# Optimization experiments

Hardware: AMD Instinct MI355X
Metric: run time of the kernel (lower is better)

## Reference

```python
import jax, jax.numpy as jnp
import numpy as np

B, T, C, H, W = 2, 8, 4, 128, 128
P = 8; D = 128; DEPTH = 2; E = 4; HD = 2 * D
Hp, Wp = H // P, W // P; F2 = 2 * D; CPP = C * P * P


def _ln(x, g, b):
    m = x.mean(-1, keepdims=True)
    v = ((x - m) ** 2).mean(-1, keepdims=True)
    return (x - m) * jax.lax.rsqrt(v + 1e-5) * g + b


def setup_inputs():
    key = jax.random.key(0)
    it = iter(jax.random.split(key, 32))
    def n(shape, s=0.02):
        return jax.random.normal(next(it), shape, jnp.float32) * s
    z = lambda shape: jnp.zeros(shape, jnp.float32)
    return {
        "x": jax.random.normal(next(it), (B, T, C, H, W), jnp.float32),
        "dt": jax.random.uniform(next(it), (T,), jnp.float32, 0.1, 1.0),
        "enc_Wre": n((CPP, D)), "enc_Wim": n((CPP, D)),
        "dec_W": n((F2, CPP)), "dec_b": z((CPP,)),
        "ln_sp_g": jnp.ones((DEPTH, F2), jnp.float32), "ln_sp_b": z((DEPTH, F2)),
        "conv_W": n((DEPTH, F2, F2, 3, 3), 0.05), "conv_b": z((DEPTH, F2)),
        "E_re": n((DEPTH, D, D), 0.05), "E_im": n((DEPTH, D, D), 0.05),
        "Dc_re": n((DEPTH, D, D), 0.05), "Dc_im": n((DEPTH, D, D), 0.05),
        "gate_W": n((DEPTH, F2, D)), "gate_b": z((DEPTH, D)),
        "src_W": n((DEPTH, F2, F2)), "src_b": z((DEPTH, F2)),
        "flux_decay": z((DEPTH, D)),
        "lam_re": n((DEPTH, D), 0.5), "lam_im": n((DEPTH, D), 0.5),
        "ln_t_g": jnp.ones((DEPTH, F2), jnp.float32), "ln_t_b": z((DEPTH, F2)),
        "rtr_W": n((DEPTH, F2, E)),
        "W1": n((DEPTH, E, F2, HD)), "b1": z((DEPTH, E, HD)),
        "W2": n((DEPTH, E, HD, F2)), "b2": z((DEPTH, E, F2)),
    }


def _forward(x, dt, enc_Wre, enc_Wim, dec_W, dec_b, ln_sp_g, ln_sp_b, conv_W, conv_b,
             E_re, E_im, Dc_re, Dc_im, gate_W, gate_b, src_W, src_b, flux_decay,
             lam_re, lam_im, ln_t_g, ln_t_b, rtr_W, W1, b1, W2, b2):
    Bx, Tx = x.shape[:2]
    # patch-embed encoder -> complex latent [B,T,D,Hp,Wp]
    f = x.reshape(Bx, Tx, C, Hp, P, Wp, P).transpose(0, 1, 3, 5, 2, 4, 6).reshape(Bx, Tx, Hp, Wp, CPP)
    zc = (f @ enc_Wre) + 1j * (f @ enc_Wim)
    zc = zc.transpose(0, 1, 4, 2, 3)
    dtBT = jnp.broadcast_to(dt[None, :], (Bx, Tx))
    flux = jnp.zeros((Bx, D), jnp.complex64)
    for i in range(DEPTH):
        # spatial branch: LayerNorm over [re,im] channels + Clifford-style 3x3 conv
        zr = jnp.concatenate([zc.real, zc.imag], axis=2).reshape(Bx * Tx, F2, Hp, Wp)
        xn = _ln(zr.transpose(0, 2, 3, 1), ln_sp_g[i], ln_sp_b[i]).transpose(0, 3, 1, 2)
        xs = jax.lax.conv_general_dilated(xn, conv_W[i], (1, 1), 'SAME',
                                          dimension_numbers=('NCHW', 'OIHW', 'NCHW')) + conv_b[i][None, :, None, None]
        sre, sim = jnp.split(xs, 2, axis=1)
        zc = zc + (sre + 1j * sim).reshape(Bx, Tx, D, Hp, Wp)
        # eigen-basis encode (complex channel mixing)
        xe = zc.transpose(0, 1, 3, 4, 2) @ (E_re[i] + 1j * E_im[i])  # B,T,Hp,Wp,D
        xm = xe.mean(axis=(2, 3))  # B,T,D complex
        # sequential flux tracker: inherently recurrent -> lax.scan over T
        gW, gb, sW, sb = gate_W[i], gate_b[i], src_W[i], src_b[i]
        dec = jax.nn.sigmoid(flux_decay[i])
        def step(fl, xmt):
            inp = jnp.concatenate([xmt.real, xmt.imag], -1)
            gate = jax.nn.sigmoid(inp @ gW + gb)
            s2 = inp @ sW + sb
            src = s2[..., :D] + 1j * s2[..., D:]
            fn = dec * fl + gate * xmt + (1.0 - gate) * src
            return fn, (fn, src)
        flux, (flux_seq, src_seq) = jax.lax.scan(step, flux, xm.transpose(1, 0, 2))
        flux_seq = flux_seq.transpose(1, 0, 2)
        src_seq = src_seq.transpose(1, 0, 2)
        g = jax.nn.sigmoid(jnp.concatenate([flux_seq.real, flux_seq.imag], -1) @ gW + gb)[:, :, None, None, :]
        forcing = xe * g + src_seq[:, :, None, None, :] * (1.0 - g)
        # complex transition operators (ZOH-style discretization)
        lam = -jax.nn.softplus(lam_re[i]) + 1j * lam_im[i]  # [D]
        opd = jnp.exp(dtBT[:, :, None] * lam[None, None, :])  # B,T,D complex
        opf = (opd - 1.0) / lam
        u = forcing * opf[:, :, None, None, :]
        A = jnp.broadcast_to(opd[:, :, None, None, :], u.shape)
        def comb(a, b):
            aA, aX = a
            bA, bX = b
            return (aA * bA, bX + bA * aX)
        # parallel pscan over time: h_t = A_t*h_{t-1} + u_t, independent per (B,Hp,Wp)
        _, uo = jax.lax.associative_scan(comb, (A, u), axis=1)
        xo = uo @ (Dc_re[i] + 1j * Dc_im[i])  # basis decode, B,T,Hp,Wp,D
        xon = _ln(jnp.concatenate([xo.real, xo.imag], -1), ln_t_g[i], ln_t_b[i])
        xcc = xon[..., :D] + 1j * xon[..., D:]
        # MoE FFN with soft routing over experts
        ft = jnp.concatenate([xcc.real, xcc.imag], -1).reshape(-1, F2)  # [M,2D]
        gates = jax.nn.softmax(ft @ rtr_W[i], axis=-1)  # [M,E]
        hmid = jax.nn.gelu(jnp.einsum('mf,efh->emh', ft, W1[i]) + b1[i][:, None, :])
        oexp = jnp.einsum('emh,ehf->emf', hmid, W2[i]) + b2[i][:, None, :]
        dtok = jnp.einsum('me,emf->mf', gates, oexp).reshape(Bx, Tx, Hp, Wp, F2)
        delta = dtok[..., :D] + 1j * dtok[..., D:]
        zc = zc + (xcc + delta).transpose(0, 1, 4, 2, 3)
    # decoder: project [re,im] -> pixels and unpatchify (real output)
    zl = zc.transpose(0, 1, 3, 4, 2)
    fo = jnp.concatenate([zl.real, zl.imag], -1) @ dec_W + dec_b
    return fo.reshape(Bx, Tx, Hp, Wp, C, P, P).transpose(0, 1, 4, 2, 5, 3, 6).reshape(Bx, Tx, C, H, W)


def reference(x, dt, enc_Wre, enc_Wim, dec_W, dec_b, ln_sp_g, ln_sp_b, conv_W, conv_b,
              E_re, E_im, Dc_re, Dc_im, gate_W, gate_b, src_W, src_b, flux_decay,
              lam_re, lam_im, ln_t_g, ln_t_b, rtr_W, W1, b1, W2, b2):
    return _forward(x, dt, enc_Wre, enc_Wim, dec_W, dec_b, ln_sp_g, ln_sp_b, conv_W, conv_b,
                    E_re, E_im, Dc_re, Dc_im, gate_W, gate_b, src_W, src_b, flux_decay,
                    lam_re, lam_im, ln_t_g, ln_t_b, rtr_W, W1, b1, W2, b2)
```

## Files before the change

### kernel.cpp

```cpp
#include <hip/hip_runtime.h>
#include <hip/hip_bf16.h>
#include <math.h>


#define NIN 28
typedef unsigned short u16;
typedef __attribute__((ext_vector_type(8))) short bf16x8;
typedef __attribute__((ext_vector_type(4))) float f32x4;
typedef __attribute__((ext_vector_type(8))) unsigned short us8;

__device__ __forceinline__ float b2f(u16 u){ union{unsigned i;float f;}v; v.i=((unsigned)u)<<16; return v.f; }
__device__ __forceinline__ u16 f2b(float x){ __hip_bfloat16 h=__float2bfloat16(x); return *(u16*)&h; }
__device__ __forceinline__ float loadraw(const void* p, size_t i, int bf){
  return bf? b2f(((const u16*)p)[i]) : ((const float*)p)[i];
}
__device__ __forceinline__ int bfflag(const void* p){ return *(const unsigned*)p==0x3F803F80u; }
__device__ __forceinline__ float d_sigmoid(float x){ return 1.0f/(1.0f+expf(-x)); }
__device__ __forceinline__ float d_softplus(float x){ return fmaxf(x,0.0f)+log1pf(expf(-fabsf(x))); }
__device__ __forceinline__ float d_gelu(float x){
  const float c=0.7978845608028654f;
  return 0.5f*x*(1.0f+tanhf(c*(x+0.044715f*x*x*x)));
}

#define NF32 17
struct MP {
  const void* src[NIN];
  int f32dst[NF32]; int f32cum[NF32+1];
  int seg[6];
};

__global__ __launch_bounds__(256) void mega_prep(MP a, float* __restrict__ W,
    u16* __restrict__ encB, u16* __restrict__ decB, u16* __restrict__ convB,
    u16* __restrict__ cplxB, u16* __restrict__ w1B, u16* __restrict__ w2c){
  const int bf=bfflag(a.src[6]);
  const int tid=threadIdx.x;
  if(blockIdx.x<512){
    __shared__ float lds[2304];
    int io=blockIdx.x;
    size_t base=(size_t)io*2304;
    for(int r=tid;r<2304;r+=256) lds[r]=loadraw(a.src[8], base+r, bf);
    __syncthreads();
    for(int k=tid;k<2304;k+=256){
      int ic=k&255, kg=k>>8;
      convB[base+k]=f2b(lds[ic*9+kg]);
    }
    return;
  }
  int g=(blockIdx.x-512)*256+tid;
  if(g>=a.seg[5]) return;
  if(g<a.seg[0]){
    int i=0;
    while(i<NF32-1 && g>=a.f32cum[i+1]) i++;
    int local=g-a.f32cum[i];
    const int needs[NF32]={1,5,6,7,9,14,15,16,17,18,19,20,21,22,23,25,27};
    W[a.f32dst[i]+local]=loadraw(a.src[needs[i]], local, bf);
  } else if(g<a.seg[1]){
    int idx=g-a.seg[0]; int n=idx>>8, k=idx&255;
    float v=(n<128)? loadraw(a.src[2],(size_t)k*128+n,bf) : loadraw(a.src[3],(size_t)k*128+(n-128),bf);
    encB[idx]=f2b(v);
  } else if(g<a.seg[2]){
    int idx=g-a.seg[1]; int n=idx>>8, k=idx&255;
    decB[idx]=f2b(loadraw(a.src[4],(size_t)k*256+n,bf));
  } else if(g<a.seg[3]){
    int idx=g-a.seg[2];
    int mat=idx>>16; int r=idx&65535; int n=r>>8, k=r&255;
    int depth=mat&1; int isD=mat>>1;
    const void* re=isD? a.src[12]:a.src[10];
    const void* im=isD? a.src[13]:a.src[11];
    size_t base=(size_t)depth*16384;
    float v;
    if(k<128){ v = (n<128)? loadraw(re,base+(size_t)k*128+n,bf) : loadraw(im,base+(size_t)k*128+(n-128),bf); }
    else{ int kk=k-128;
      v = (n<128)? -loadraw(im,base+(size_t)kk*128+n,bf) : loadraw(re,base+(size_t)kk*128+(n-128),bf); }
    cplxB[idx]=f2b(v);
  } else if(g<a.seg[4]){
    int idx=g-a.seg[3]; int m=idx>>16; int r=idx&65535; int n=r>>8, k=r&255;
    w1B[idx]=f2b(loadraw(a.src[24],(size_t)m*65536+(size_t)k*256+n,bf));
  } else {
    int idx=g-a.seg[4];
    int i=idx>>18; int r=idx&262143; int n=r>>10; int k=r&1023;
    int e=k>>8, h=k&255;
    size_t s=(((size_t)(i*4+e)*256+h)*256+n);
    w2c[idx]=f2b(loadraw(a.src[26],s,bf));
  }
}

#define FB_BIAS 1
#define FB_GELU 2
#define FB_RS 4
#define FB_ADDTO 8
#define FB_WF32 16
#define FB_WBF16 32
#define FB_CONV 64
#define FB_MOE2 256
#define FB_UNPATCH 512
#define FB_XM 1024

template<int FLAGS>
__global__ __launch_bounds__(256,4) void mfma_gemm(
    const void* __restrict__ Asrc, const u16* __restrict__ Bt,
    const float* __restrict__ bias, const float* __restrict__ gates,
    float* __restrict__ Cf, u16* __restrict__ Cb,
    const u16* __restrict__ Xtra, void* __restrict__ Cout, const void* __restrict__ flagp,
    int K, long aE, long bE, long biasE, long cE, long cRow,
    float* __restrict__ xm4)
{
  __shared__ u16 As[2][64][72];
  __shared__ u16 Bs[2][64][72];
  const int e=blockIdx.z;
  const u16* A=(const u16*)Asrc + (size_t)e*aE;
  Bt += (size_t)e*bE;
  const float* biasp = bias? bias+(size_t)e*biasE : nullptr;
  const int bn=blockIdx.x*64, bm=blockIdx.y*64;
  const int tid=threadIdx.x, l=tid&63, w=tid>>6;
  const int wm=w&1, wn=w>>1;
  int bf=0;
  if(FLAGS&FB_UNPATCH) bf=bfflag(flagp);
  const us8 z8={0,0,0,0,0,0,0,0};

  auto loadAi=[&](int k0, int i)->us8{
    int c=tid+(i<<8); int row=c>>3, col8=(c&7)<<3;
    int gk=k0+col8;
    if(FLAGS&FB_CONV){
      int m=bm+row; int bt=m>>8, rem=m&255, hp=rem>>4, wp=rem&15;
      int kg=gk>>8, ic=gk&255; int ky=kg/3, kx=kg-3*ky;
      int y=hp+ky-1, x=wp+kx-1;
      return ((unsigned)y<16u && (unsigned)x<16u)?
           *(const us8*)&A[(((size_t)(bt*16+y))*16+x)*256+ic] : z8;
    }
    return *(const us8*)&A[(size_t)(bm+row)*K+gk];
  };
  auto loadBi=[&](int k0, int i)->us8{
    int c=tid+(i<<8); int row=c>>3, col8=(c&7)<<3;
    return *(const us8*)&Bt[(size_t)(bn+row)*K+k0+col8];
  };

  us8 ra0,ra1,rb0,rb1;
  ra0=loadAi(0,0); ra1=loadAi(0,1); rb0=loadBi(0,0); rb1=loadBi(0,1);
  {
    int c0=tid, c1=tid+256;
    *(us8*)&As[0][c0>>3][(c0&7)<<3]=ra0;
    *(us8*)&As[0][c1>>3][(c1&7)<<3]=ra1;
    *(us8*)&Bs[0][c0>>3][(c0&7)<<3]=rb0;
    *(us8*)&Bs[0][c1>>3][(c1&7)<<3]=rb1;
  }
  const int kSteps=K>>6;
  if(kSteps>1){ ra0=loadAi(64,0); ra1=loadAi(64,1); rb0=loadBi(64,0); rb1=loadBi(64,1); }
  __syncthreads();

  f32x4 zf={0.f,0.f,0.f,0.f};
  f32x4 acc00=zf, acc01=zf, acc10=zf, acc11=zf;
  const int aRow0=wm*32+(l&15), bRow0=wn*32+(l&15);
  const int kcL=(l>>4)<<3;

  for(int ks=0; ks<kSteps; ++ks){
    const int cur=ks&1;
    if(ks+1<kSteps){
      int nb=cur^1;
      int c0=tid, c1=tid+256;
      *(us8*)&As[nb][c0>>3][(c0&7)<<3]=ra0;
      *(us8*)&As[nb][c1>>3][(c1&7)<<3]=ra1;
      *(us8*)&Bs[nb][c0>>3][(c0&7)<<3]=rb0;
      *(us8*)&Bs[nb][c1>>3][(c1&7)<<3]=rb1;
      if(ks+2<kSteps){
        int k0=(ks+2)<<6;
        ra0=loadAi(k0,0); ra1=loadAi(k0,1); rb0=loadBi(k0,0); rb1=loadBi(k0,1);
      }
    }
    #pragma unroll
    for(int kk=0;kk<64;kk+=32){
      const int kc=kk+kcL;
      bf16x8 a0=*(const bf16x8*)&As[cur][aRow0   ][kc];
      bf16x8 a1=*(const bf16x8*)&As[cur][aRow0+16][kc];
      bf16x8 b0=*(const bf16x8*)&Bs[cur][bRow0   ][kc];
      bf16x8 b1=*(const bf16x8*)&Bs[cur][bRow0+16][kc];
      acc00=__builtin_amdgcn_mfma_f32_16x16x32_bf16(a0,b0,acc00,0,0,0);
      acc01=__builtin_amdgcn_mfma_f32_16x16x32_bf16(a0,b1,acc01,0,0,0);
      acc10=__builtin_amdgcn_mfma_f32_16x16x32_bf16(a1,b0,acc10,0,0,0);
      acc11=__builtin_amdgcn_mfma_f32_16x16x32_bf16(a1,b1,acc11,0,0,0);
    }
    __syncthreads();
  }

  const int rr=(l>>4)<<2, cc=l&15;
  #pragma unroll
  for(int mi=0;mi<2;mi++){
    #pragma unroll
    for(int ni=0;ni<2;ni++){
      f32x4 av = mi? (ni?acc11:acc10) : (ni?acc01:acc00);
      #pragma unroll
      for(int r=0;r<4;r++){
        int m=bm+wm*32+mi*16+rr+r;
        int n=bn+wn*32+ni*16+cc;
        float v=av[r];
        if(FLAGS&FB_BIAS) v+=biasp[n];
        if(FLAGS&FB_GELU) v=d_gelu(v);
        if(FLAGS&FB_RS)   v*=gates[(size_t)m*4+e];
        if(FLAGS&FB_MOE2){
          #pragma unroll
          for(int ee=0;ee<4;ee++) v+=gates[(size_t)m*4+ee]*bias[ee*256+n];
          v+=b2f(Xtra[(size_t)m*256+n]);
        }
        if(FLAGS&FB_UNPATCH){
          int bt=m>>8, hp=(m>>4)&15, wp=m&15;
          int c=n>>6, ph=(n>>3)&7, pw=n&7;
          size_t o=((size_t)bt<<16)|((size_t)c<<14)|((size_t)(hp*8+ph)<<7)|(size_t)(wp*8+pw);
          if(bf) ((__hip_bfloat16*)Cout)[o]=__float2bfloat16(v);
          else   ((float*)Cout)[o]=v;
          continue;
        }
        size_t o=(size_t)e*cE + (size_t)m*cRow + n;
        if(FLAGS&FB_ADDTO) v+=Cf[o];
        if(FLAGS&(FB_WF32|FB_ADDTO)) Cf[o]=v;
        if(FLAGS&FB_WBF16) Cb[o]=f2b(v);
      }
    }
  }

  if(FLAGS&FB_XM){
    float cs0=acc00[0]+acc00[1]+acc00[2]+acc00[3] + acc10[0]+acc10[1]+acc10[2]+acc10[3];
    float cs1=acc01[0]+acc01[1]+acc01[2]+acc01[3] + acc11[0]+acc11[1]+acc11[2]+acc11[3];
    cs0+=__shfl_xor(cs0,16); cs0+=__shfl_xor(cs0,32);
    cs1+=__shfl_xor(cs1,16); cs1+=__shfl_xor(cs1,32);
    float* xr=(float*)&As[0][0][0];
    if(l<16){
      xr[wm*64 + wn*32 + cc]      = cs0;
      xr[wm*64 + wn*32 + 16 + cc] = cs1;
    }
    __syncthreads();
    if(tid<64){
      float s=xr[tid]+xr[64+tid];
      xm4[(size_t)blockIdx.y*256 + bn + tid]=s;
    }
  }
}

#define FR_GATHER 1
#define FR_WF32 2
#define FR_MOE2 4
#define FR_ADDTO 8
#define FR_LN 16
#define FR_RTR 32

template<int FLAGS>
__global__ __launch_bounds__(256) void gemm_fullrow(
    const void* __restrict__ Asrc, const u16* __restrict__ Bt,
    const float* __restrict__ b2, const float* __restrict__ gatesIn,
    float* __restrict__ Cf, const u16* __restrict__ Xtra,
    const float* __restrict__ lnG, const float* __restrict__ lnB, u16* __restrict__ lnOut,
    const float* __restrict__ rtr, float* __restrict__ gatesOut,
    const void* __restrict__ flagp, int K)
{
  __shared__ u16 As[2][16][72];
  __shared__ u16 Bs[2][256][72];
  __shared__ float sc[480];
  const int bm=blockIdx.x*16;
  const int tid=threadIdx.x, l=tid&63, w=tid>>6;
  int bf=0;
  if(FLAGS&FR_GATHER) bf=bfflag(flagp);
  const bool aAct = tid<128;

  auto loadA=[&](int k0)->us8{
    int row=tid>>3, col8=(tid&7)<<3;
    int gk=k0+col8;
    if(FLAGS&FR_GATHER){
      int m=bm+row; int bt=m>>8, rem=m&255, hp=rem>>4, wp=rem&15;
      int c2=gk>>6, ph=(gk>>3)&7;
      size_t sidx=(((size_t)bt*4+c2)<<14)+(size_t)((hp*8+ph)<<7)+wp*8;
      if(bf) return *(const us8*)&((const u16*)Asrc)[sidx];
      const float* xf=(const float*)Asrc+sidx;
      us8 t;
      #pragma unroll
      for(int j=0;j<8;j++) t[j]=f2b(xf[j]);
      return t;
    }
    return *(const us8*)&((const u16*)Asrc)[(size_t)(bm+row)*K+gk];
  };
  auto loadB=[&](int k0, int j)->us8{
    int c=tid+(j<<8); int row=c>>3, col8=(c&7)<<3;
    return *(const us8*)&Bt[(size_t)row*K+k0+col8];
  };

  us8 ra, rb[8];
  if(aAct) ra=loadA(0);
  #pragma unroll
  for(int j=0;j<8;j++) rb[j]=loadB(0,j);
  if(aAct) *(us8*)&As[0][tid>>3][(tid&7)<<3]=ra;
  #pragma unroll
  for(int j=0;j<8;j++){ int c=tid+(j<<8); *(us8*)&Bs[0][c>>3][(c&7)<<3]=rb[j]; }
  const int kSteps=K>>6;
  if(kSteps>1){ if(aAct) ra=loadA(64); 
    #pragma unroll
    for(int j=0;j<8;j++) rb[j]=loadB(64,j); }
  __syncthreads();

  f32x4 zf={0.f,0.f,0.f,0.f};
  f32x4 acc[4]={zf,zf,zf,zf};
  const int kcL=(l>>4)<<3;

  for(int ks=0; ks<kSteps; ++ks){
    const int cur=ks&1;
    if(ks+1<kSteps){
      int nb=cur^1;
      if(aAct) *(us8*)&As[nb][tid>>3][(tid&7)<<3]=ra;
      #pragma unroll
      for(int j=0;j<8;j++){ int c=tid+(j<<8); *(us8*)&Bs[nb][c>>3][(c&7)<<3]=rb[j]; }
      if(ks+2<kSteps){
        int k0=(ks+2)<<6;
        if(aAct) ra=loadA(k0);
        #pragma unroll
        for(int j=0;j<8;j++) rb[j]=loadB(k0,j);
      }
    }
    #pragma unroll
    for(int kk=0;kk<64;kk+=32){
      const int kc=kk+kcL;
      bf16x8 a=*(const bf16x8*)&As[cur][l&15][kc];
      #pragma unroll
      for(int ni=0;ni<4;ni++){
        bf16x8 b=*(const bf16x8*)&Bs[cur][w*64+ni*16+(l&15)][kc];
        acc[ni]=__builtin_amdgcn_mfma_f32_16x16x32_bf16(a,b,acc[ni],0,0,0);
      }
    }
    __syncthreads();
  }

  const int rr=(l>>4)<<2, cc=l&15;
  float v[4][4];
  #pragma unroll
  for(int ni=0;ni<4;ni++){
    #pragma unroll
    for(int r=0;r<4;r++){
      int m=bm+rr+r, n=w*64+ni*16+cc;
      float x=acc[ni][r];
      if(FLAGS&FR_MOE2){
        #pragma unroll
        for(int ee=0;ee<4;ee++) x+=gatesIn[(size_t)m*4+ee]*b2[ee*256+n];
        x+=b2f(Xtra[(size_t)m*256+n]);
      }
      size_t o=(size_t)m*256+n;
      if(FLAGS&FR_ADDTO) x+=Cf[o];
      if(FLAGS&(FR_WF32|FR_ADDTO)) Cf[o]=x;
      v[ni][r]=x;
    }
  }

  if(FLAGS&FR_LN){
    float rs[4]={0,0,0,0}, rq[4]={0,0,0,0};
    #pragma unroll
    for(int ni=0;ni<4;ni++)
      #pragma unroll
      for(int r=0;r<4;r++){ rs[r]+=v[ni][r]; rq[r]+=v[ni][r]*v[ni][r]; }
    #pragma unroll
    for(int o=1;o<16;o<<=1){
      #pragma unroll
      for(int r=0;r<4;r++){ rs[r]+=__shfl_xor(rs[r],o); rq[r]+=__shfl_xor(rq[r],o); }
    }
    if((l&15)==0){
      int q=l>>4;
      #pragma unroll
      for(int r=0;r<4;r++){ sc[w*16+q*4+r]=rs[r]; sc[64+w*16+q*4+r]=rq[r]; }
    }
    __syncthreads();
    if(tid<16){
      float tot=0,tq=0;
      #pragma unroll
      for(int w4=0;w4<4;w4++){ tot+=sc[w4*16+tid]; tq+=sc[64+w4*16+tid]; }
      float mean=tot*(1.0f/256.0f);
      float var=tq*(1.0f/256.0f)-mean*mean;
      sc[128+tid]=mean; sc[144+tid]=rsqrtf(var+1e-5f);
    }
    __syncthreads();
    float nvv[4][4];
    #pragma unroll
    for(int ni=0;ni<4;ni++)
      #pragma unroll
      for(int r=0;r<4;r++){
        int row=rr+r, n=w*64+ni*16+cc;
        float nv=(v[ni][r]-sc[128+row])*sc[144+row]*lnG[n]+lnB[n];
        nvv[ni][r]=nv;
        lnOut[(size_t)(bm+row)*256+n]=f2b(nv);
      }
    if(FLAGS&FR_RTR){
      float pe[4][4]={{0,0,0,0},{0,0,0,0},{0,0,0,0},{0,0,0,0}};
      #pragma unroll
      for(int ni=0;ni<4;ni++){
        int n=w*64+ni*16+cc;
        #pragma unroll
        for(int r=0;r<4;r++)
          #pragma unroll
          for(int e=0;e<4;e++) pe[r][e]+=nvv[ni][r]*rtr[n*4+e];
      }
      #pragma unroll
      for(int o=1;o<16;o<<=1)
        #pragma unroll
        for(int r=0;r<4;r++)
          #pragma unroll
          for(int e=0;e<4;e++) pe[r][e]+=__shfl_xor(pe[r][e],o);
      if((l&15)==0){
        int q=l>>4;
        #pragma unroll
        for(int r=0;r<4;r++)
          #pragma unroll
          for(int e=0;e<4;e++) sc[160+w*64+(q*4+r)*4+e]=pe[r][e];
      }
      __syncthreads();
      if(tid<64){
        int row=tid>>2, e=tid&3;
        float t=0;
        #pragma unroll
        for(int w4=0;w4<4;w4++) t+=sc[160+w4*64+row*4+e];
        sc[416+row*4+e]=t;
      }
      __syncthreads();
      if(tid<16){
        float a0=sc[416+tid*4],a1=sc[416+tid*4+1],a2=sc[416+tid*4+2],a3=sc[416+tid*4+3];
        float mx=fmaxf(fmaxf(a0,a1),fmaxf(a2,a3));
        float e0=expf(a0-mx),e1=expf(a1-mx),e2=expf(a2-mx),e3=expf(a3-mx);
        float inv=1.0f/(e0+e1+e2+e3);
        gatesOut[(size_t)(bm+tid)*4+0]=e0*inv;
        gatesOut[(size_t)(bm+tid)*4+1]=e1*inv;
        gatesOut[(size_t)(bm+tid)*4+2]=e2*inv;
        gatesOut[(size_t)(bm+tid)*4+3]=e3*inv;
      }
    }
  }
}

__global__ __launch_bounds__(384) void gate_src_k(const float* __restrict__ xm4,
    const float* __restrict__ sW, const float* __restrict__ sb,
    const float* __restrict__ gW, const float* __restrict__ gb,
    float* __restrict__ xm, float* __restrict__ s2, float* __restrict__ gt,
    const float* __restrict__ dt, const float* __restrict__ lam_re, const float* __restrict__ lam_im,
    float* __restrict__ odr_, float* __restrict__ odi_, float* __restrict__ ofr_, float* __restrict__ ofi_){
  int tid=threadIdx.x;
  if(blockIdx.x==16){
    for(int idx=tid; idx<1024; idx+=384){
      int t=idx>>7, d=idx&127;
      float lr=-d_softplus(lam_re[d]);
      float li=lam_im[d];
      float dtv=dt[t];
      float er=expf(dtv*lr);
      float odr=er*cosf(dtv*li), odi=er*sinf(dtv*li);
      float den=lr*lr+li*li;
      float ar=odr-1.0f, ai=odi;
      odr_[idx]=odr; odi_[idx]=odi;
      ofr_[idx]=(ar*lr+ai*li)/den;
      ofi_[idx]=(ai*lr-ar*li)/den;
    }
    return;
  }
  int bt=blockIdx.x;
  __shared__ float inp[256];
  if(tid<256){
    int rb=bt*4;
    float v=(xm4[(size_t)rb*256+tid]+xm4[(size_t)(rb+1)*256+tid]
            +xm4[(size_t)(rb+2)*256+tid]+xm4[(size_t)(rb+3)*256+tid])*(1.0f/256.0f);
    inp[tid]=v; xm[bt*256+tid]=v;
  }
  __syncthreads();
  if(tid<256){
    float acc=sb[tid];
    #pragma unroll 8
    for(int k=0;k<256;k++) acc+=inp[k]*sW[k*256+tid];
    s2[bt*256+tid]=acc;
  }else{
    int d=tid-256;
    float acc=gb[d];
    #pragma unroll 8
    for(int k=0;k<256;k++) acc+=inp[k]*gW[k*128+d];
    gt[bt*128+d]=d_sigmoid(acc);
  }
}

__global__ __launch_bounds__(128) void flux_gate2(const float* __restrict__ xm,
    const float* __restrict__ s2, const float* __restrict__ gt,
    const float* __restrict__ fdec, const float* __restrict__ fbin, float* __restrict__ fbout,
    const float* __restrict__ gW, const float* __restrict__ gb, float* __restrict__ gbuf, int init){
  int bt=blockIdx.x; int b=bt>>3, t=bt&7; int d=threadIdx.x;
  float flr = init? 0.f : fbin[b*256+d];
  float fli = init? 0.f : fbin[b*256+128+d];
  float dec = d_sigmoid(fdec[d]);
  for(int tp=0; tp<=t; tp++){
    int q=b*8+tp;
    float gv=gt[q*128+d];
    flr = dec*flr + gv*xm[q*256+d]     + (1.0f-gv)*s2[q*256+d];
    fli = dec*fli + gv*xm[q*256+128+d] + (1.0f-gv)*s2[q*256+128+d];
  }
  __shared__ float inp[256];
  inp[d]=flr; inp[128+d]=fli;
  __syncthreads();
  float acc=gb[d];
  #pragma unroll 8
  for(int k=0;k<256;k++) acc+=inp[k]*gW[k*128+d];
  gbuf[bt*128+d]=d_sigmoid(acc);
  if(t==7){ fbout[b*256+d]=flr; fbout[b*256+128+d]=fli; }
}

__global__ __launch_bounds__(256) void fscan_t(const float* __restrict__ xe,
    const float* __restrict__ gbuf, const float* __restrict__ ss,
    const float* __restrict__ odr, const float* __restrict__ odi,
    const float* __restrict__ ofr, const float* __restrict__ ofi, u16* __restrict__ uo){
  int idx=blockIdx.x*256+threadIdx.x;
  int d=idx&127, s=(idx>>7)&255, b=idx>>15;
  float hr=0.f, hi=0.f;
  for(int t=0;t<8;t++){
    int bt=b*8+t;
    size_t n=(size_t)bt*256+s;
    float g=gbuf[bt*128+d];
    float sr=ss[bt*256+d], si=ss[bt*256+128+d];
    float xr=xe[n*256+d], xi=xe[n*256+128+d];
    float fr=xr*g+sr*(1.0f-g), fi=xi*g+si*(1.0f-g);
    float pr=ofr[t*128+d], pi=ofi[t*128+d];
    float ur=fr*pr-fi*pi, ui=fr*pi+fi*pr;
    float ar=odr[t*128+d], ai=odi[t*128+d];
    float nr=ar*hr-ai*hi+ur, ni=ar*hi+ai*hr+ui;
    hr=nr; hi=ni;
    uo[n*256+d]=f2b(hr); uo[n*256+128+d]=f2b(hi);
  }
}

extern "C" void kernel_launch(void* const* d_in, const int* in_sizes, int n_in,
                              void* d_out, int out_size, void* d_ws, size_t ws_size,
                              hipStream_t stream){
  (void)out_size; (void)ws_size; (void)n_in;
  int acum[NIN+1]; acum[0]=0;
  for(int i=0;i<NIN;i++) acum[i+1]=acum[i]+((i==0)?0:in_sizes[i]);
  const int totalA=acum[NIN];
  float* W=(float*)d_ws;
  size_t off=((size_t)totalA+63)&~(size_t)63;
  float* zc  =W+off; off+=1048576;
  float* xe  =W+off; off+=1048576;
  u16* zcb =(u16*)(W+off); off+=524288;
  u16* xnb =(u16*)(W+off); off+=524288;
  u16* uob =(u16*)(W+off); off+=524288;
  u16* ftb =(u16*)(W+off); off+=524288;
  u16* hmid=(u16*)(W+off); off+=2097152;
  u16* encB=(u16*)(W+off); off+=32768;
  u16* decB=(u16*)(W+off); off+=32768;
  u16* convB=(u16*)(W+off); off+=589824;
  u16* cplxB=(u16*)(W+off); off+=131072;
  u16* w1B =(u16*)(W+off); off+=262144;
  u16* w2c =(u16*)(W+off); off+=262144;
  float* xm4 =W+off; off+=16384;
  float* xm  =W+off; off+=4096;
  float* s2  =W+off; off+=4096;
  float* gt  =W+off; off+=2048;
  float* gbuf=W+off; off+=2048;
  float* odr =W+off; off+=1024;
  float* odi =W+off; off+=1024;
  float* ofr =W+off; off+=1024;
  float* ofi =W+off; off+=1024;
  float* gates=W+off; off+=16384;
  float* fbA =W+off; off+=512;
  float* fbB =W+off; off+=512;

  MP mp;
  for(int i=0;i<NIN;i++) mp.src[i]=d_in[i];
  const int needs[NF32]={1,5,6,7,9,14,15,16,17,18,19,20,21,22,23,25,27};
  mp.f32cum[0]=0;
  for(int j=0;j<NF32;j++){ mp.f32cum[j+1]=mp.f32cum[j]+in_sizes[needs[j]]; mp.f32dst[j]=acum[needs[j]]; }
  mp.seg[0]=mp.f32cum[NF32];
  mp.seg[1]=mp.seg[0]+65536;
  mp.seg[2]=mp.seg[1]+65536;
  mp.seg[3]=mp.seg[2]+262144;
  mp.seg[4]=mp.seg[3]+524288;
  mp.seg[5]=mp.seg[4]+524288;
  int restBlocks=(mp.seg[5]+255)/256;
  mega_prep<<<512+restBlocks,256,0,stream>>>(mp, W, encB, decB, convB, cplxB, w1B, w2c);

  const dim3 GG(4,64,1);
  const float* lnspg0=W+acum[6];

  gemm_fullrow<FR_GATHER|FR_WF32|FR_LN><<<256,256,0,stream>>>(d_in[0], encB,
      nullptr, nullptr, zc, nullptr,
      W+acum[6]+0*256, W+acum[7]+0*256, xnb, nullptr, nullptr, d_in[6], 256);

  for(int i=0;i<2;i++){
    const float* convb=W+acum[9]+i*256;
    const float* gWp  =W+acum[14]+i*32768;
    const float* gbp  =W+acum[15]+i*128;
    const float* sWp  =W+acum[16]+i*65536;
    const float* sbp  =W+acum[17]+i*256;
    const float* fdec =W+acum[18]+i*128;
    const float* lamre=W+acum[19]+i*128;
    const float* lamim=W+acum[20]+i*128;
    const float* lntg =W+acum[21]+i*256;
    const float* lntb =W+acum[22]+i*256;
    const float* rtr  =W+acum[23]+i*1024;
    const float* b1   =W+acum[25]+i*1024;
    const float* b2   =W+acum[27]+i*1024;

    mfma_gemm<FB_CONV|FB_BIAS|FB_ADDTO|FB_WBF16><<<GG,256,0,stream>>>(xnb, convB+(size_t)i*589824,
        convb, nullptr, zc, zcb, nullptr, nullptr, nullptr, 2304, 0,0,0,0,256, nullptr);
    mfma_gemm<FB_WF32|FB_XM><<<GG,256,0,stream>>>(zcb, cplxB+(size_t)i*65536, nullptr, nullptr,
        xe, nullptr, nullptr, nullptr, nullptr, 256, 0,0,0,0,256, xm4);
    gate_src_k<<<17,384,0,stream>>>(xm4, sWp, sbp, gWp, gbp, xm, s2, gt,
        W+acum[1], lamre, lamim, odr, odi, ofr, ofi);
    flux_gate2<<<16,128,0,stream>>>(xm, s2, gt, fdec, (i==0)?nullptr:fbA, (i==0)?fbA:fbB,
        gWp, gbp, gbuf, (i==0)?1:0);
    fscan_t<<<256,256,0,stream>>>(xe, gbuf, s2, odr, odi, ofr, ofi, uob);
    gemm_fullrow<FR_LN|FR_RTR><<<256,256,0,stream>>>(uob, cplxB+(size_t)(2+i)*65536,
        nullptr, nullptr, nullptr, nullptr,
        lntg, lntb, ftb, rtr, gates, nullptr, 256);
    mfma_gemm<FB_BIAS|FB_GELU|FB_RS|FB_WBF16><<<dim3(4,64,4),256,0,stream>>>(ftb, w1B+(size_t)i*262144,
        b1, gates, nullptr, hmid, nullptr, nullptr, nullptr, 256, 0,65536,256,256,1024, nullptr);
    if(i==0){
      gemm_fullrow<FR_MOE2|FR_ADDTO|FR_WF32|FR_LN><<<256,256,0,stream>>>(hmid, w2c,
          b2, gates, zc, ftb,
          W+acum[6]+1*256, W+acum[7]+1*256, xnb, nullptr, nullptr, nullptr, 1024);
    }else{
      mfma_gemm<FB_MOE2|FB_ADDTO|FB_WBF16><<<GG,256,0,stream>>>(hmid, w2c+262144,
          b2, gates, zc, zcb, ftb, nullptr, nullptr, 1024, 0,0,0,0,256, nullptr);
    }
  }

  mfma_gemm<FB_BIAS|FB_UNPATCH><<<GG,256,0,stream>>>(zcb, decB, W+acum[5], nullptr,
      nullptr, nullptr, nullptr, d_out, d_in[6], 256, 0,0,0,0,256, nullptr);
}
```

Baseline: 191.8 us.

## Fuse flux recurrence, gate, time scan and decoder GEMM with LN/router

After: 227.8 us. 18.8% more time.

```diff
diff --git a/kernel.cpp b/kernel.cpp
--- a/kernel.cpp
+++ b/kernel.cpp
@@ -4,6 +4,7 @@
 
 
 #define NIN 28
+#define NF32 17
 typedef unsigned short u16;
 typedef __attribute__((ext_vector_type(8))) short bf16x8;
 typedef __attribute__((ext_vector_type(4))) float f32x4;
@@ -22,7 +23,6 @@
   return 0.5f*x*(1.0f+tanhf(c*(x+0.044715f*x*x*x)));
 }
 
-#define NF32 17
 struct MP {
   const void* src[NIN];
   int f32dst[NF32]; int f32cum[NF32+1];
@@ -222,6 +222,7 @@
     float cs1=acc01[0]+acc01[1]+acc01[2]+acc01[3] + acc11[0]+acc11[1]+acc11[2]+acc11[3];
     cs0+=__shfl_xor(cs0,16); cs0+=__shfl_xor(cs0,32);
     cs1+=__shfl_xor(cs1,16); cs1+=__shfl_xor(cs1,32);
+    __syncthreads();
     float* xr=(float*)&As[0][0][0];
     if(l<16){
       xr[wm*64 + wn*32 + cc]      = cs0;
@@ -289,7 +290,7 @@
   #pragma unroll
   for(int j=0;j<8;j++){ int c=tid+(j<<8); *(us8*)&Bs[0][c>>3][(c&7)<<3]=rb[j]; }
   const int kSteps=K>>6;
-  if(kSteps>1){ if(aAct) ra=loadA(64); 
+  if(kSteps>1){ if(aAct) ra=loadA(64);
     #pragma unroll
     for(int j=0;j<8;j++) rb[j]=loadB(64,j); }
   __syncthreads();
@@ -473,50 +474,185 @@
   }
 }
 
-__global__ __launch_bounds__(128) void flux_gate2(const float* __restrict__ xm,
-    const float* __restrict__ s2, const float* __restrict__ gt,
+__global__ __launch_bounds__(256) void dec_fused(
+    const float* __restrict__ xe, const float* __restrict__ xm,
+    const float* __restrict__ s2g, const float* __restrict__ gtg,
     const float* __restrict__ fdec, const float* __restrict__ fbin, float* __restrict__ fbout,
-    const float* __restrict__ gW, const float* __restrict__ gb, float* __restrict__ gbuf, int init){
-  int bt=blockIdx.x; int b=bt>>3, t=bt&7; int d=threadIdx.x;
-  float flr = init? 0.f : fbin[b*256+d];
-  float fli = init? 0.f : fbin[b*256+128+d];
-  float dec = d_sigmoid(fdec[d]);
-  for(int tp=0; tp<=t; tp++){
-    int q=b*8+tp;
-    float gv=gt[q*128+d];
-    flr = dec*flr + gv*xm[q*256+d]     + (1.0f-gv)*s2[q*256+d];
-    fli = dec*fli + gv*xm[q*256+128+d] + (1.0f-gv)*s2[q*256+128+d];
-  }
-  __shared__ float inp[256];
-  inp[d]=flr; inp[128+d]=fli;
-  __syncthreads();
-  float acc=gb[d];
-  #pragma unroll 8
-  for(int k=0;k<256;k++) acc+=inp[k]*gW[k*128+d];
-  gbuf[bt*128+d]=d_sigmoid(acc);
-  if(t==7){ fbout[b*256+d]=flr; fbout[b*256+128+d]=fli; }
-}
-
-__global__ __launch_bounds__(256) void fscan_t(const float* __restrict__ xe,
-    const float* __restrict__ gbuf, const float* __restrict__ ss,
+    const float* __restrict__ gW, const float* __restrict__ gb,
     const float* __restrict__ odr, const float* __restrict__ odi,
-    const float* __restrict__ ofr, const float* __restrict__ ofi, u16* __restrict__ uo){
-  int idx=blockIdx.x*256+threadIdx.x;
-  int d=idx&127, s=(idx>>7)&255, b=idx>>15;
-  float hr=0.f, hi=0.f;
-  for(int t=0;t<8;t++){
-    int bt=b*8+t;
-    size_t n=(size_t)bt*256+s;
-    float g=gbuf[bt*128+d];
-    float sr=ss[bt*256+d], si=ss[bt*256+128+d];
-    float xr=xe[n*256+d], xi=xe[n*256+128+d];
-    float fr=xr*g+sr*(1.0f-g), fi=xi*g+si*(1.0f-g);
-    float pr=ofr[t*128+d], pi=ofi[t*128+d];
-    float ur=fr*pr-fi*pi, ui=fr*pi+fi*pr;
-    float ar=odr[t*128+d], ai=odi[t*128+d];
-    float nr=ar*hr-ai*hi+ur, ni=ar*hi+ai*hr+ui;
-    hr=nr; hi=ni;
-    uo[n*256+d]=f2b(hr); uo[n*256+128+d]=f2b(hi);
+    const float* __restrict__ ofr, const float* __restrict__ ofi,
+    const u16* __restrict__ Bt, const float* __restrict__ lnG, const float* __restrict__ lnB,
+    u16* __restrict__ ftb, const float* __restrict__ rtr, float* __restrict__ gates, int init)
+{
+  __shared__ u16 uoLDS[16][264];
+  __shared__ float sc[480];
+  __shared__ union {
+    struct { float fseq[8][256]; float gbufL[8][128]; } pre;
+    u16 Bs[256][72];
+  } su;
+  const int blk=blockIdx.x;
+  const int bt=blk>>4, b=bt>>3, t=bt&7, hp=blk&15;
+  const int tid=threadIdx.x, l=tid&63, w=tid>>6;
+
+  {
+    int d=tid&127, im=tid>>7;
+    float fl = init? 0.f : fbin[b*256+im*128+d];
+    float dec = d_sigmoid(fdec[d]);
+    for(int tp=0; tp<=t; tp++){
+      int q=b*8+tp;
+      float gv=gtg[q*128+d];
+      fl = dec*fl + gv*xm[q*256+im*128+d] + (1.0f-gv)*s2g[q*256+im*128+d];
+      su.pre.fseq[tp][im*128+d]=fl;
+    }
+    if(t==7) fbout[b*256+im*128+d]=fl;
+  }
+  __syncthreads();
+  for(int idx=tid; idx<(t+1)*128; idx+=256){
+    int tp=idx>>7, d2=idx&127;
+    float acc=gb[d2];
+    #pragma unroll 8
+    for(int k=0;k<256;k++) acc+=su.pre.fseq[tp][k]*gW[k*128+d2];
+    su.pre.gbufL[tp][d2]=d_sigmoid(acc);
+  }
+  __syncthreads();
+  for(int u=tid; u<2048; u+=256){
+    int wp=u>>7, d=u&127;
+    int s=hp*16+wp;
+    float hr=0.f, hi=0.f;
+    for(int tp=0; tp<=t; tp++){
+      int bt2=b*8+tp;
+      size_t n2=(size_t)bt2*256+s;
+      float g=su.pre.gbufL[tp][d];
+      float sr=s2g[bt2*256+d], si=s2g[bt2*256+128+d];
+      float xr=xe[n2*256+d], xi=xe[n2*256+128+d];
+      float fr=xr*g+sr*(1.0f-g), fi=xi*g+si*(1.0f-g);
+      float pr=ofr[tp*128+d], pi=ofi[tp*128+d];
+      float ur=fr*pr-fi*pi, ui=fr*pi+fi*pr;
+      float ar=odr[tp*128+d], ai=odi[tp*128+d];
+      float nr=ar*hr-ai*hi+ur, ni=ar*hi+ai*hr+ui;
+      hr=nr; hi=ni;
+    }
+    uoLDS[wp][d]=f2b(hr); uoLDS[wp][128+d]=f2b(hi);
+  }
+  __syncthreads();
+
+  auto loadB=[&](int k0, int j)->us8{
+    int c=tid+(j<<8); int row=c>>3, col8=(c&7)<<3;
+    return *(const us8*)&Bt[(size_t)row*256+k0+col8];
+  };
+  us8 rb[8];
+  #pragma unroll
+  for(int j=0;j<8;j++) rb[j]=loadB(0,j);
+
+  f32x4 zf={0.f,0.f,0.f,0.f};
+  f32x4 acc[4]={zf,zf,zf,zf};
+  const int kcL=(l>>4)<<3;
+  for(int ks=0; ks<4; ++ks){
+    __syncthreads();
+    #pragma unroll
+    for(int j=0;j<8;j++){ int c=tid+(j<<8); *(us8*)&su.Bs[c>>3][(c&7)<<3]=rb[j]; }
+    if(ks<3){
+      int k0=(ks+1)<<6;
+      #pragma unroll
+      for(int j=0;j<8;j++) rb[j]=loadB(k0,j);
+    }
+    __syncthreads();
+    #pragma unroll
+    for(int kk=0;kk<64;kk+=32){
+      const int kc=kk+kcL;
+      bf16x8 a=*(const bf16x8*)&uoLDS[l&15][(ks<<6)+kc];
+      #pragma unroll
+      for(int ni=0;ni<4;ni++){
+        bf16x8 bb=*(const bf16x8*)&su.Bs[w*64+ni*16+(l&15)][kc];
+        acc[ni]=__builtin_amdgcn_mfma_f32_16x16x32_bf16(a,bb,acc[ni],0,0,0);
+      }
+    }
+  }
+
+  const int rr=(l>>4)<<2, cc=l&15;
+  const int bm=blk*16;
+  float v[4][4];
+  #pragma unroll
+  for(int ni=0;ni<4;ni++)
+    #pragma unroll
+    for(int r=0;r<4;r++) v[ni][r]=acc[ni][r];
+
+  float rs[4]={0,0,0,0}, rq[4]={0,0,0,0};
+  #pragma unroll
+  for(int ni=0;ni<4;ni++)
+    #pragma unroll
+    for(int r=0;r<4;r++){ rs[r]+=v[ni][r]; rq[r]+=v[ni][r]*v[ni][r]; }
+  #pragma unroll
+  for(int o=1;o<16;o<<=1){
+    #pragma unroll
+    for(int r=0;r<4;r++){ rs[r]+=__shfl_xor(rs[r],o); rq[r]+=__shfl_xor(rq[r],o); }
+  }
+  __syncthreads();
+  if((l&15)==0){
+    int q=l>>4;
+    #pragma unroll
+    for(int r=0;r<4;r++){ sc[w*16+q*4+r]=rs[r]; sc[64+w*16+q*4+r]=rq[r]; }
+  }
+  __syncthreads();
+  if(tid<16){
+    float tot=0,tq=0;
+    #pragma unroll
+    for(int w4=0;w4<4;w4++){ tot+=sc[w4*16+tid]; tq+=sc[64+w4*16+tid]; }
+    float mean=tot*(1.0f/256.0f);
+    float var=tq*(1.0f/256.0f)-mean*mean;
+    sc[128+tid]=mean; sc[144+tid]=rsqrtf(var+1e-5f);
+  }
+  __syncthreads();
+  float nvv[4][4];
+  #pragma unroll
+  for(int ni=0;ni<4;ni++)
+    #pragma unroll
+    for(int r=0;r<4;r++){
+      int row=rr+r, n=w*64+ni*16+cc;
+      float nv=(v[ni][r]-sc[128+row])*sc[144+row]*lnG[n]+lnB[n];
+      nvv[ni][r]=nv;
+      ftb[(size_t)(bm+row)*256+n]=f2b(nv);
+    }
+  float pe[4][4]={{0,0,0,0},{0,0,0,0},{0,0,0,0},{0,0,0,0}};
+  #pragma unroll
+  for(int ni=0;ni<4;ni++){
+    int n=w*64+ni*16+cc;
+    #pragma unroll
+    for(int r=0;r<4;r++)
+      #pragma unroll
+      for(int e=0;e<4;e++) pe[r][e]+=nvv[ni][r]*rtr[n*4+e];
+  }
+  #pragma unroll
+  for(int o=1;o<16;o<<=1)
+    #pragma unroll
+    for(int r=0;r<4;r++)
+      #pragma unroll
+      for(int e=0;e<4;e++) pe[r][e]+=__shfl_xor(pe[r][e],o);
+  if((l&15)==0){
+    int q=l>>4;
+    #pragma unroll
+    for(int r=0;r<4;r++)
+      #pragma unroll
+      for(int e=0;e<4;e++) sc[160+w*64+(q*4+r)*4+e]=pe[r][e];
+  }
+  __syncthreads();
+  if(tid<64){
+    int row=tid>>2, e=tid&3;
+    float tt=0;
+    #pragma unroll
+    for(int w4=0;w4<4;w4++) tt+=sc[160+w4*64+row*4+e];
+    sc[416+row*4+e]=tt;
+  }
+  __syncthreads();
+  if(tid<16){
+    float a0=sc[416+tid*4],a1=sc[416+tid*4+1],a2=sc[416+tid*4+2],a3=sc[416+tid*4+3];
+    float mx=fmaxf(fmaxf(a0,a1),fmaxf(a2,a3));
+    float e0=expf(a0-mx),e1=expf(a1-mx),e2=expf(a2-mx),e3=expf(a3-mx);
+    float inv=1.0f/(e0+e1+e2+e3);
+    gates[(size_t)(bm+tid)*4+0]=e0*inv;
+    gates[(size_t)(bm+tid)*4+1]=e1*inv;
+    gates[(size_t)(bm+tid)*4+2]=e2*inv;
+    gates[(size_t)(bm+tid)*4+3]=e3*inv;
   }
 }
 
@@ -533,7 +669,6 @@
   float* xe  =W+off; off+=1048576;
   u16* zcb =(u16*)(W+off); off+=524288;
   u16* xnb =(u16*)(W+off); off+=524288;
-  u16* uob =(u16*)(W+off); off+=524288;
   u16* ftb =(u16*)(W+off); off+=524288;
   u16* hmid=(u16*)(W+off); off+=2097152;
   u16* encB=(u16*)(W+off); off+=32768;
@@ -546,7 +681,6 @@
   float* xm  =W+off; off+=4096;
   float* s2  =W+off; off+=4096;
   float* gt  =W+off; off+=2048;
-  float* gbuf=W+off; off+=2048;
   float* odr =W+off; off+=1024;
   float* odi =W+off; off+=1024;
   float* ofr =W+off; off+=1024;
@@ -570,7 +704,6 @@
   mega_prep<<<512+restBlocks,256,0,stream>>>(mp, W, encB, decB, convB, cplxB, w1B, w2c);
 
   const dim3 GG(4,64,1);
-  const float* lnspg0=W+acum[6];
 
   gemm_fullrow<FR_GATHER|FR_WF32|FR_LN><<<256,256,0,stream>>>(d_in[0], encB,
       nullptr, nullptr, zc, nullptr,
@@ -597,12 +730,10 @@
         xe, nullptr, nullptr, nullptr, nullptr, 256, 0,0,0,0,256, xm4);
     gate_src_k<<<17,384,0,stream>>>(xm4, sWp, sbp, gWp, gbp, xm, s2, gt,
         W+acum[1], lamre, lamim, odr, odi, ofr, ofi);
-    flux_gate2<<<16,128,0,stream>>>(xm, s2, gt, fdec, (i==0)?nullptr:fbA, (i==0)?fbA:fbB,
-        gWp, gbp, gbuf, (i==0)?1:0);
-    fscan_t<<<256,256,0,stream>>>(xe, gbuf, s2, odr, odi, ofr, ofi, uob);
-    gemm_fullrow<FR_LN|FR_RTR><<<256,256,0,stream>>>(uob, cplxB+(size_t)(2+i)*65536,
-        nullptr, nullptr, nullptr, nullptr,
-        lntg, lntb, ftb, rtr, gates, nullptr, 256);
+    dec_fused<<<256,256,0,stream>>>(xe, xm, s2, gt, fdec,
+        (i==0)? nullptr : fbA, (i==0)? fbA : fbB,
+        gWp, gbp, odr, odi, ofr, ofi,
+        cplxB+(size_t)(2+i)*65536, lntg, lntb, ftb, rtr, gates, (i==0)?1:0);
     mfma_gemm<FB_BIAS|FB_GELU|FB_RS|FB_WBF16><<<dim3(4,64,4),256,0,stream>>>(ftb, w1B+(size_t)i*262144,
         b1, gates, nullptr, hmid, nullptr, nullptr, nullptr, 256, 0,65536,256,256,1024, nullptr);
     if(i==0){
```
